# Optimization experiments

Hardware: AMD Instinct MI355X
Metric: run time of the kernel (lower is better)

Reference implementation:

```python
import jax, jax.numpy as jnp
import numpy as np

HIDDEN = 256
HEAD = 256
GAMMA = 0.96875
SCALE_BASE = 512  # default scale_base in the standard XPOS module


def xpos_apply(x, offset=0, downscale=False):
    """xpos rotary embedding. x: (B, S, H) with H even."""
    B, S, H = x.shape
    half = H // 2
    dt = x.dtype
    pos = jnp.arange(offset, offset + S, dtype=dt)  # (S,)
    # per-channel xpos scale: ((2i + 0.4H) / (1.4H)) ** (pos / scale_base)
    base_scale = (jnp.arange(0, H, 2, dtype=dt) + 0.4 * H) / (1.4 * H)  # (half,)
    scale = base_scale[None, :] ** (pos[:, None] / SCALE_BASE)          # (S, half)
    if downscale:
        scale = 1.0 / scale
    inv_freq = 1.0 / (10000.0 ** (jnp.arange(half, dtype=dt) / half))   # (half,)
    sinusoid = pos[:, None] * inv_freq[None, :]                         # (S, half)
    sin = jnp.sin(sinusoid) * scale
    cos = jnp.cos(sinusoid) * scale
    # duplicate-interleave columns to width H
    sin2 = jnp.repeat(sin, 2, axis=-1)  # (S, H)
    cos2 = jnp.repeat(cos, 2, axis=-1)
    # rotate_every_two
    x1 = x[..., 0::2]
    x2 = x[..., 1::2]
    rot = jnp.stack([-x2, x1], axis=-1).reshape(x.shape)
    return x * cos2[None] + rot * sin2[None]


def decay_mask(S, dtype):
    n = jnp.arange(S)
    diff = n[:, None] - n[None, :]
    # gamma^(i-j) for i>=j else 0 (clamp exponent to avoid huge values under the mask)
    D = jnp.where(diff >= 0,
                  jnp.asarray(GAMMA, dtype) ** jnp.maximum(diff, 0).astype(dtype),
                  jnp.zeros((), dtype))
    return D


def setup_inputs() -> dict:
    key = jax.random.key(0)
    k1, k2, k3, k4 = jax.random.split(key, 4)
    B, N, S = 2, 8, 2048
    X = jax.random.normal(k1, (B, N, S, HIDDEN), dtype=jnp.float32)
    # kaiming-uniform-ish init: uniform in [-1/sqrt(fan_in), 1/sqrt(fan_in)]
    bound = 1.0 / np.sqrt(HIDDEN)
    W_Q = jax.random.uniform(k2, (HIDDEN, HEAD), jnp.float32, -bound, bound)
    W_K = jax.random.uniform(k3, (HIDDEN, HEAD), jnp.float32, -bound, bound)
    W_V = jax.random.uniform(k4, (HIDDEN, HEAD), jnp.float32, -bound, bound)
    return {"X": X, "W_Q": W_Q, "W_K": W_K, "W_V": W_V}


def reference(X, W_Q, W_K, W_V):
    B, N, S, H = X.shape
    Q = X @ W_Q  # (B, N, S, head)
    K = X @ W_K
    V = X @ W_V
    hd = Q.shape[-1]
    Q = xpos_apply(Q.reshape(B * N, S, hd)).reshape(B, N, S, hd)
    K = xpos_apply(K.reshape(B * N, S, hd), downscale=True).reshape(B, N, S, hd)
    D = decay_mask(S, X.dtype)  # (S, S)
    scores = jnp.einsum('bnsh,bnth->bnst', Q, K) * D  # (B, N, S, S)
    return scores @ V  # (B, N, S, v_dim)
```

## Files before the change

kernel.cpp:

```cpp
#include <hip/hip_runtime.h>
#include <hip/hip_bf16.h>


#define S_LEN 2048
#define HD 256
#define BN 16

typedef _Float16 half8 __attribute__((ext_vector_type(8)));
typedef _Float16 half4 __attribute__((ext_vector_type(4)));
typedef _Float16 half2v __attribute__((ext_vector_type(2)));
typedef float floatx16 __attribute__((ext_vector_type(16)));

__device__ __forceinline__ void gl_lds16(const void* g, void* l) {
  __builtin_amdgcn_global_load_lds(
      (const __attribute__((address_space(1))) unsigned int*)(unsigned long long)g,
      (__attribute__((address_space(3))) unsigned int*)(unsigned int)(unsigned long long)l,
      16, 0, 0);
}

__global__ __launch_bounds__(256) void prep_kernel(
    const float* __restrict__ WQ, const float* __restrict__ WK,
    const float* __restrict__ WV, _Float16* __restrict__ WT,
    _Float16* __restrict__ TBL) {
  const int b = blockIdx.x;
  const int tid = threadIdx.x;
  if (b < 1024) {
    const int idx = b * 256 + tid;
    const int i2 = idx & 127;
    const int pos = idx >> 7;
    float inv_freq = exp2f(-(float)i2 * (13.287712379549449f / 128.0f));
    float lbase = log2f(((float)(2 * i2) + 102.4f) / 358.4f);
    float ang = (float)pos * inv_freq;
    float sn, cs;
    sincosf(ang, &sn, &cs);
    float scl = exp2f((float)pos * (1.0f / 512.0f) * lbase);
    float rscl = 1.0f / scl;
    half2v tq, tk;
    tq[0] = (_Float16)(cs * scl);  tq[1] = (_Float16)(sn * scl);
    tk[0] = (_Float16)(cs * rscl); tk[1] = (_Float16)(sn * rscl);
    *(half2v*)&TBL[(long)idx * 2] = tq;
    *(half2v*)&TBL[(long)(262144 + idx) * 2] = tk;
    return;
  }
  __shared__ _Float16 trans[64][72];
  const int bb = b - 1024;
  const int w = bb >> 4;
  const int tk = ((bb & 15) & 3) * 64;
  const int tn = ((bb & 15) >> 2) * 64;
  const float* W = (w == 0) ? WQ : (w == 1) ? WK : WV;
#pragma unroll
  for (int u = 0; u < 4; ++u) {
    int idx = u * 256 + tid;
    int k = idx >> 4;
    int nq = (idx & 15) * 4;
    float4 v = *(const float4*)&W[(tk + k) * HD + tn + nq];
    trans[nq + 0][k] = (_Float16)v.x;
    trans[nq + 1][k] = (_Float16)v.y;
    trans[nq + 2][k] = (_Float16)v.z;
    trans[nq + 3][k] = (_Float16)v.w;
  }
  __syncthreads();
#pragma unroll
  for (int u = 0; u < 2; ++u) {
    int idx = u * 256 + tid;
    int n = idx >> 3;
    int kq = (idx & 7) * 8;
    *(uint4*)&WT[((long)w * HD + tn + n) * HD + tk + kq] = *(const uint4*)&trans[n][kq];
  }
}

__global__ __launch_bounds__(256) void gemm_qkv_kernel(
    const float* __restrict__ X, const _Float16* __restrict__ WT,
    const _Float16* __restrict__ TBL,
    _Float16* __restrict__ Q, _Float16* __restrict__ K,
    _Float16* __restrict__ VT) {
  __shared__ __align__(16) unsigned char smem[66560];
  unsigned char* ep = smem + 32768;

  const int tid = threadIdx.x;
  const int lane = tid & 63;
  const int w = tid >> 6;
  const int l31 = lane & 31;
  const int lh = lane >> 5;
  const int m0 = blockIdx.x * 64;
  const int mtile = w & 1;
  const int nhalf = w >> 1;

#pragma unroll
  for (int i = 0; i < 8; ++i) {
    int id = i * 256 + tid;
    int row = id >> 5, c = id & 31;
    int p = c ^ (row & 31);
    const float4* s = (const float4*)&X[(long)(m0 + row) * HD + c * 8];
    float4 v0 = s[0], v1 = s[1];
    half8 h;
    h[0] = (_Float16)v0.x; h[1] = (_Float16)v0.y;
    h[2] = (_Float16)v0.z; h[3] = (_Float16)v0.w;
    h[4] = (_Float16)v1.x; h[5] = (_Float16)v1.y;
    h[6] = (_Float16)v1.z; h[7] = (_Float16)v1.w;
    *(half8*)(smem + row * 512 + p * 16) = h;
  }
  __syncthreads();

  const int bn = m0 >> 11;
  const int srow0 = m0 & (S_LEN - 1);
  const int mrow = mtile * 32 + l31;
  const int nbase = nhalf * 128;

  for (int wsel = 0; wsel < 3; ++wsel) {
    const _Float16* Wb = WT + (long)wsel * HD * HD;
    floatx16 acc[4];
#pragma unroll
    for (int nt = 0; nt < 4; ++nt)
#pragma unroll
      for (int e = 0; e < 16; ++e) acc[nt][e] = 0.f;

    half8 b[5][4];
#pragma unroll
    for (int pk = 0; pk < 5; ++pk)
#pragma unroll
      for (int nt = 0; nt < 4; ++nt)
        b[pk][nt] = *(const half8*)(Wb + (long)(nbase + nt * 32 + l31) * HD +
                                    pk * 16 + lh * 8);
#pragma unroll
    for (int ks16 = 0; ks16 < 16; ++ks16) {
      const int slot = ks16 % 5;
      int p = (ks16 * 2 + lh) ^ l31;
      half8 af = *(const half8*)(smem + mrow * 512 + p * 16);
#pragma unroll
      for (int nt = 0; nt < 4; ++nt)
        acc[nt] = __builtin_amdgcn_mfma_f32_32x32x16_f16(af, b[slot][nt], acc[nt], 0, 0, 0);
      if (ks16 + 5 < 16) {
#pragma unroll
        for (int nt = 0; nt < 4; ++nt)
          b[slot][nt] = *(const half8*)(Wb + (long)(nbase + nt * 32 + l31) * HD +
                                        (ks16 + 5) * 16 + lh * 8);
      }
    }

    if (wsel < 2) {
#pragma unroll
      for (int nt = 0; nt < 4; ++nt) {
        int col = nbase + nt * 32 + l31;
#pragma unroll
        for (int reg = 0; reg < 16; ++reg) {
          int rmap = (reg & 3) + 8 * (reg >> 2) + 4 * lh;
          *(_Float16*)(ep + (mtile * 32 + rmap) * 528 + col * 2) =
              (_Float16)acc[nt][reg];
        }
      }
      __syncthreads();
      _Float16* o = wsel ? K : Q;
      const _Float16* tb_base = TBL + (long)wsel * 2048 * 128 * 2;
#pragma unroll
      for (int u = 0; u < 8; ++u) {
        int id = u * 256 + tid;
        int row = id >> 5;
        int cq = (id & 31) * 8;
        half8 x = *(const half8*)(ep + row * 528 + cq * 2);
        half8 t = *(const half8*)&tb_base[((long)(srow0 + row) * 128 + (cq >> 1)) * 2];
        half8 y;
        y[0] = x[0] * t[0] - x[1] * t[1];
        y[1] = x[1] * t[0] + x[0] * t[1];
        y[2] = x[2] * t[2] - x[3] * t[3];
        y[3] = x[3] * t[2] + x[2] * t[3];
        y[4] = x[4] * t[4] - x[5] * t[5];
        y[5] = x[5] * t[4] + x[4] * t[5];
        y[6] = x[6] * t[6] - x[7] * t[7];
        y[7] = x[7] * t[6] + x[6] * t[7];
        *(half8*)&o[(long)(m0 + row) * HD + cq] = y;
      }
      __syncthreads();
    } else {
      __syncthreads();
      _Float16 (*vt)[72] = (_Float16(*)[72])smem;
#pragma unroll
      for (int nt = 0; nt < 4; ++nt) {
        int h = nbase + nt * 32 + l31;
#pragma unroll
        for (int reg = 0; reg < 16; ++reg) {
          int rmap = (reg & 3) + 8 * (reg >> 2) + 4 * lh;
          vt[h][mtile * 32 + rmap] = (_Float16)acc[nt][reg];
        }
      }
      __syncthreads();
#pragma unroll
      for (int u = 0; u < 8; ++u) {
        int id = u * 256 + tid;
        int h = id >> 3, sj = (id & 7) * 8;
        *(uint4*)&VT[((long)bn * HD + h) * S_LEN + srow0 + sj] = *(const uint4*)&vt[h][sj];
      }
    }
  }
}

__global__ __launch_bounds__(256) void retention_kernel(
    const _Float16* __restrict__ Q, const _Float16* __restrict__ K,
    const _Float16* __restrict__ VT, float* __restrict__ out) {
  __shared__ __align__(16) unsigned char smem[74752];
  unsigned char* ksb = smem;
  unsigned char* vsb = smem + 32768;
  _Float16 (*sc)[72] = (_Float16(*)[72])(smem + 65536);

  const int tid = threadIdx.x;
  const int lane = tid & 63;
  const int w = tid >> 6;
  const int l31 = lane & 31;
  const int lh = lane >> 5;
  const int qtile = w >> 1;
  const int ttile = w & 1;
  const int hhalf = w & 1;

  const int L = blockIdx.x;
  const int head = L & 15;
  const int qt = 31 - (L >> 4);
  const int q0 = qt * 64;

  const _Float16* Qh = Q + (long)head * S_LEN * HD;
  const _Float16* Kh = K + (long)head * S_LEN * HD;
  const _Float16* VTh = VT + (long)head * HD * S_LEN;

  half8 qf[16];
  {
    const _Float16* qrow = Qh + (long)(q0 + qtile * 32 + l31) * HD + lh * 8;
#pragma unroll
    for (int ks16 = 0; ks16 < 16; ++ks16)
      qf[ks16] = *(const half8*)(qrow + ks16 * 16);
  }

  floatx16 acc[4];
#pragma unroll
  for (int nt = 0; nt < 4; ++nt)
#pragma unroll
    for (int e = 0; e < 16; ++e) acc[nt][e] = 0.f;

  const float LG = -0.0458036896f;
  float Cg[16];
#pragma unroll
  for (int g = 0; g < 4; ++g)
#pragma unroll
    for (int r = 0; r < 4; ++r) Cg[4 * g + r] = exp2f(-(float)(8 * g + r) * LG);

  const int kst_row = (w * 8) * 2;
#define STAGE_K(T0)                                                        \
  {                                                                        \
    _Pragma("unroll") for (int j = 0; j < 8; ++j) {                        \
      int li = w * 8 + j;                                                  \
      int row = li * 2 + lh;                                               \
      int c = l31 ^ (row & 31);                                            \
      gl_lds16(Kh + (long)((T0) + row) * HD + c * 8, ksb + li * 1024);     \
    }                                                                      \
  }
#define STAGE_V(T0)                                                        \
  {                                                                        \
    _Pragma("unroll") for (int j = 0; j < 8; ++j) {                        \
      int li = w * 8 + j;                                                  \
      int row = li * 8 + (lane >> 3);                                      \
      int c = (lane & 7) ^ (row & 7);                                      \
      gl_lds16(VTh + (long)row * S_LEN + (T0) + c * 8, vsb + li * 1024);   \
    }                                                                      \
  }

  (void)kst_row;
  STAGE_K(0);
  STAGE_V(0);

  for (int kt = 0; kt <= qt; ++kt) {
    const int t0 = kt * 64;
    __syncthreads();

    floatx16 s;
#pragma unroll
    for (int e = 0; e < 16; ++e) s[e] = 0.f;
    {
      const unsigned char* kbase = ksb + (ttile * 32 + l31) * 512;
#pragma unroll
      for (int ks16 = 0; ks16 < 16; ++ks16) {
        int p = (ks16 * 2 + lh) ^ l31;
        half8 a = *(const half8*)(kbase + p * 16);
        s = __builtin_amdgcn_mfma_f32_32x32x16_f16(a, qf[ks16], s, 0, 0, 0);
      }
    }

    {
      const int qg = q0 + qtile * 32 + l31;
      const int tb = t0 + ttile * 32 + 4 * lh;
      const int dd = qg - tb;
      const float E = exp2f((float)dd * LG);
#pragma unroll
      for (int g = 0; g < 4; ++g) {
        half4 h4;
#pragma unroll
        for (int r = 0; r < 4; ++r) {
          int o = 8 * g + r;
          float wv = (dd >= o) ? E * Cg[4 * g + r] : 0.f;
          h4[r] = (_Float16)(s[4 * g + r] * wv);
        }
        *(half4*)&sc[qtile * 32 + l31][ttile * 32 + 4 * lh + 8 * g] = h4;
      }
    }
    __syncthreads();

    if (kt < qt) STAGE_K(t0 + 64);

#pragma unroll
    for (int kst = 0; kst < 4; ++kst) {
      half8 a = *(const half8*)&sc[qtile * 32 + l31][kst * 16 + lh * 8];
#pragma unroll
      for (int nt = 0; nt < 4; ++nt) {
        int h = hhalf * 128 + nt * 32 + l31;
        int p = (kst * 2 + lh) ^ (h & 7);
        half8 b = *(const half8*)(vsb + h * 128 + p * 16);
        acc[nt] = __builtin_amdgcn_mfma_f32_32x32x16_f16(a, b, acc[nt], 0, 0, 0);
      }
    }
    __syncthreads();

    if (kt < qt) STAGE_V(t0 + 64);
  }

  const long rbase = (long)head * S_LEN + q0 + qtile * 32;
#pragma unroll
  for (int nt = 0; nt < 4; ++nt) {
    int col = hhalf * 128 + nt * 32 + l31;
#pragma unroll
    for (int reg = 0; reg < 16; ++reg) {
      int rmap = (reg & 3) + 8 * (reg >> 2) + 4 * lh;
      out[(rbase + rmap) * HD + col] = acc[nt][reg];
    }
  }
}

extern "C" void kernel_launch(void* const* d_in, const int* in_sizes, int n_in,
                              void* d_out, int out_size, void* d_ws, size_t ws_size,
                              hipStream_t stream) {
  const float* X  = (const float*)d_in[0];
  const float* WQ = (const float*)d_in[1];
  const float* WK = (const float*)d_in[2];
  const float* WV = (const float*)d_in[3];
  float* out = (float*)d_out;

  _Float16* Qh = (_Float16*)d_ws;
  _Float16* Kh = Qh + (size_t)BN * S_LEN * HD;
  _Float16* VTh = Kh + (size_t)BN * S_LEN * HD;
  _Float16* WT = VTh + (size_t)BN * S_LEN * HD;
  _Float16* TBL = WT + (size_t)3 * HD * HD;

  prep_kernel<<<dim3(1072), dim3(256), 0, stream>>>(WQ, WK, WV, WT, TBL);
  gemm_qkv_kernel<<<dim3((BN * S_LEN) / 64), dim3(256), 0, stream>>>(
      X, WT, TBL, Qh, Kh, VTh);
  retention_kernel<<<dim3(512), dim3(256), 0, stream>>>(Qh, Kh, VTh, out);
}
```

Baseline: 191.2 us.

## Double-buffer K tiles in LDS and load V fragments directly into registers

```diff
diff --git a/kernel.cpp b/kernel.cpp
--- a/kernel.cpp
+++ b/kernel.cpp
@@ -198,8 +198,8 @@
     const _Float16* __restrict__ Q, const _Float16* __restrict__ K,
     const _Float16* __restrict__ VT, float* __restrict__ out) {
   __shared__ __align__(16) unsigned char smem[74752];
-  unsigned char* ksb = smem;
-  unsigned char* vsb = smem + 32768;
+  unsigned char* ksb0 = smem;
+  unsigned char* ksb1 = smem + 32768;
   _Float16 (*sc)[72] = (_Float16(*)[72])(smem + 65536);
 
   const int tid = threadIdx.x;
@@ -213,7 +213,8 @@
 
   const int L = blockIdx.x;
   const int head = L & 15;
-  const int qt = 31 - (L >> 4);
+  const int j = (L >> 4) & 15;
+  const int qt = (L < 256) ? (31 - j) : j;
   const int q0 = qt * 64;
 
   const _Float16* Qh = Q + (long)head * S_LEN * HD;
@@ -241,39 +242,40 @@
 #pragma unroll
     for (int r = 0; r < 4; ++r) Cg[4 * g + r] = exp2f(-(float)(8 * g + r) * LG);
 
-  const int kst_row = (w * 8) * 2;
-#define STAGE_K(T0)                                                        \
+#define STAGE_K(T0, DST)                                                   \
   {                                                                        \
-    _Pragma("unroll") for (int j = 0; j < 8; ++j) {                        \
-      int li = w * 8 + j;                                                  \
+    _Pragma("unroll") for (int jj = 0; jj < 8; ++jj) {                     \
+      int li = w * 8 + jj;                                                 \
       int row = li * 2 + lh;                                               \
       int c = l31 ^ (row & 31);                                            \
-      gl_lds16(Kh + (long)((T0) + row) * HD + c * 8, ksb + li * 1024);     \
+      gl_lds16(Kh + (long)((T0) + row) * HD + c * 8, (DST) + li * 1024);   \
     }                                                                      \
   }
-#define STAGE_V(T0)                                                        \
-  {                                                                        \
-    _Pragma("unroll") for (int j = 0; j < 8; ++j) {                        \
-      int li = w * 8 + j;                                                  \
-      int row = li * 8 + (lane >> 3);                                      \
-      int c = (lane & 7) ^ (row & 7);                                      \
-      gl_lds16(VTh + (long)row * S_LEN + (T0) + c * 8, vsb + li * 1024);   \
-    }                                                                      \
-  }
-
-  (void)kst_row;
-  STAGE_K(0);
-  STAGE_V(0);
+
+  STAGE_K(0, ksb0);
 
   for (int kt = 0; kt <= qt; ++kt) {
     const int t0 = kt * 64;
+    unsigned char* kcur = (kt & 1) ? ksb1 : ksb0;
+    unsigned char* knxt = (kt & 1) ? ksb0 : ksb1;
+
     __syncthreads();
+
+    if (kt < qt) STAGE_K(t0 + 64, knxt);
+
+    half8 vb[4][4];
+#pragma unroll
+    for (int kst = 0; kst < 4; ++kst)
+#pragma unroll
+      for (int nt = 0; nt < 4; ++nt)
+        vb[kst][nt] = *(const half8*)(VTh +
+            (long)(hhalf * 128 + nt * 32 + l31) * S_LEN + t0 + kst * 16 + lh * 8);
 
     floatx16 s;
 #pragma unroll
     for (int e = 0; e < 16; ++e) s[e] = 0.f;
     {
-      const unsigned char* kbase = ksb + (ttile * 32 + l31) * 512;
+      const unsigned char* kbase = kcur + (ttile * 32 + l31) * 512;
 #pragma unroll
       for (int ks16 = 0; ks16 < 16; ++ks16) {
         int p = (ks16 * 2 + lh) ^ l31;
@@ -299,24 +301,18 @@
         *(half4*)&sc[qtile * 32 + l31][ttile * 32 + 4 * lh + 8 * g] = h4;
       }
     }
-    __syncthreads();
-
-    if (kt < qt) STAGE_K(t0 + 64);
+
+    asm volatile("s_waitcnt lgkmcnt(0)" ::: "memory");
+    __builtin_amdgcn_s_barrier();
+    asm volatile("" ::: "memory");
 
 #pragma unroll
     for (int kst = 0; kst < 4; ++kst) {
       half8 a = *(const half8*)&sc[qtile * 32 + l31][kst * 16 + lh * 8];
 #pragma unroll
-      for (int nt = 0; nt < 4; ++nt) {
-        int h = hhalf * 128 + nt * 32 + l31;
-        int p = (kst * 2 + lh) ^ (h & 7);
-        half8 b = *(const half8*)(vsb + h * 128 + p * 16);
-        acc[nt] = __builtin_amdgcn_mfma_f32_32x32x16_f16(a, b, acc[nt], 0, 0, 0);
-      }
-    }
-    __syncthreads();
-
-    if (kt < qt) STAGE_V(t0 + 64);
+      for (int nt = 0; nt < 4; ++nt)
+        acc[nt] = __builtin_amdgcn_mfma_f32_32x32x16_f16(a, vb[kst][nt], acc[nt], 0, 0, 0);
+    }
   }
 
   const long rbase = (long)head * S_LEN + q0 + qtile * 32;
```

Result: slower. 251.6 us (+31.6%).
